# Optimization experiments

Measured on AMD Instinct MI355X. Metric: run time of the kernel, lower is better.

Reference implementation:

```python
import jax, jax.numpy as jnp
import numpy as np

B, N, D, H, DH, DEPTH = 4, 1024, 1024, 16, 64, 4
FI = int(D * 4.0 * 2 / 3)  # 2730, GEGLU inner dim
EPS = 1.1920929e-07  # torch float32 eps (RMSNorm default)
NEG = -jnp.finfo(jnp.float32).max


def rms(x, w):
    return x * jax.lax.rsqrt(jnp.mean(x * x, axis=-1, keepdims=True) + EPS) * w


def rope(t):
    # t: [b, h, n, d]; interleaved-pair rotary (lucidrains rotary_embedding_torch)
    n, d = t.shape[-2], t.shape[-1]
    inv_freq = 1.0 / (10000.0 ** (jnp.arange(0, d, 2, dtype=jnp.float32) / d))
    ang = jnp.arange(n, dtype=jnp.float32)[:, None] * inv_freq  # [n, d/2]
    cos = jnp.repeat(jnp.cos(ang), 2, axis=-1)  # [n, d]
    sin = jnp.repeat(jnp.sin(ang), 2, axis=-1)
    x = t.reshape(t.shape[:-1] + (d // 2, 2))
    rot = jnp.stack([-x[..., 1], x[..., 0]], axis=-1).reshape(t.shape)
    return t * cos + rot * sin


def setup_inputs() -> dict:
    key = jax.random.key(0)
    ks = jax.random.split(key, 14)
    s = 0.02
    return {
        "x": jax.random.normal(ks[0], (B, N, D), dtype=jnp.float32),
        "norm_attn_w": jnp.ones((DEPTH, D), jnp.float32),
        "wq": jax.random.normal(ks[1], (DEPTH, H * DH, D), jnp.float32) * s,
        "wkv": jax.random.normal(ks[2], (DEPTH, 2 * H * DH, D), jnp.float32) * s,
        "wo": jax.random.normal(ks[3], (DEPTH, D, H * DH), jnp.float32) * s,
        "wg": jax.random.normal(ks[4], (DEPTH, H, D), jnp.float32) * s,
        "wmix": jax.random.normal(ks[5], (DEPTH, H, D), jnp.float32) * s,
        "norm_ff_w": jnp.ones((DEPTH, D), jnp.float32),
        "ff_norm_w": jnp.ones((DEPTH, D), jnp.float32),
        "w_in": jax.random.normal(ks[6], (DEPTH, 2 * FI, D), jnp.float32) * s,
        "b_in": jnp.zeros((DEPTH, 2 * FI), jnp.float32),
        "w_out": jax.random.normal(ks[7], (DEPTH, D, FI), jnp.float32) * s,
        "b_out": jnp.zeros((DEPTH, D), jnp.float32),
        "final_norm_w": jnp.ones((D,), jnp.float32),
    }


def _forward(x, norm_attn_w, wq, wkv, wo, wg, wmix, norm_ff_w, ff_norm_w,
             w_in, b_in, w_out, b_out, final_norm_w):
    scale = DH ** -0.5
    causal = jnp.triu(jnp.ones((N, N), bool), k=1)  # True = masked
    value_residual = None
    for i in range(DEPTH):
        # --- attention block (pre-RMSNorm wrapper) ---
        h = rms(x, norm_attn_w[i])  # [b, n, d]
        q = jnp.einsum('bnd,ed->bne', h, wq[i]) * scale
        kv = jnp.einsum('bnd,ed->bne', h, wkv[i])
        k, v = jnp.split(kv, 2, axis=-1)
        split = lambda t: t.reshape(B, N, H, DH).transpose(0, 2, 1, 3)  # b h n d
        q, k, v = split(q), split(k), split(v)
        orig_v = v
        if value_residual is not None:
            mix = jax.nn.sigmoid(jnp.einsum('bnd,hd->bhn', h, wmix[i]))[..., None]
            v = v + mix * (value_residual - v)  # lerp(v, value_residual, mix)
        q, k = rope(q), rope(k)
        sim = jnp.einsum('bhid,bhjd->bhij', q, k)
        sim = jnp.where(causal, NEG, sim)
        attn = jax.nn.softmax(sim, axis=-1)
        out = jnp.einsum('bhij,bhjd->bhid', attn, v)
        gates = jax.nn.sigmoid(jnp.einsum('bnd,hd->bhn', h, wg[i]))[..., None]
        out = out * gates
        out = out.transpose(0, 2, 1, 3).reshape(B, N, H * DH)
        x = x + jnp.einsum('bne,de->bnd', out, wo[i])
        if value_residual is None:
            value_residual = orig_v
        # --- feedforward block (wrapper norm + FF's own pre-rmsnorm) ---
        g = rms(x, norm_ff_w[i])
        g = rms(g, ff_norm_w[i])
        u = jnp.einsum('bnd,ed->bne', g, w_in[i]) + b_in[i]
        a, gt = jnp.split(u, 2, axis=-1)
        u = a * jax.nn.gelu(gt, approximate=False)
        x = x + jnp.einsum('bnf,df->bnd', u, w_out[i]) + b_out[i]
    return rms(x, final_norm_w)


def reference(x, norm_attn_w, wq, wkv, wo, wg, wmix, norm_ff_w, ff_norm_w,
              w_in, b_in, w_out, b_out, final_norm_w):
    return _forward(x, norm_attn_w, wq, wkv, wo, wg, wmix, norm_ff_w,
                    ff_norm_w, w_in, b_in, w_out, b_out, final_norm_w)
```

## Files before the change

kernel.cpp:

```cpp
#include <hip/hip_runtime.h>
#include <cstdint>
#include <cstddef>


#define DEV_INLINE __device__ __forceinline__

typedef short bf16x8 __attribute__((ext_vector_type(8)));
typedef float f32x4 __attribute__((ext_vector_type(4)));

constexpr int Bsz = 4, Nseq = 1024, Dm = 1024, Hh = 16, DH = 64, NDEPTH = 4;
constexpr int FI = 2730;
constexpr int FI_PAD = 2752;
constexpr int FI_TILE = 2816;
constexpr int WIDE = 2 * FI_TILE;
constexpr int ROWS = Bsz * Nseq;
constexpr float EPSR = 1.1920929e-07f;

DEV_INLINE float bf2f(unsigned short u) {
  unsigned int x = ((unsigned int)u) << 16;
  float f; __builtin_memcpy(&f, &x, 4); return f;
}
DEV_INLINE unsigned short f2bf(float f) {
  unsigned int x; __builtin_memcpy(&x, &f, 4);
  unsigned int r = x + 0x7fffu + ((x >> 16) & 1u);
  return (unsigned short)(r >> 16);
}

using gptr_t = const __attribute__((address_space(1))) void*;
using lptr_t = __attribute__((address_space(3))) void*;
DEV_INLINE void gl_lds16(const void* g, void* l) {
  __builtin_amdgcn_global_load_lds((gptr_t)g, (lptr_t)l, 16, 0, 0);
}
DEV_INLINE void fence_mem() { asm volatile("" ::: "memory"); }

__global__ __launch_bounds__(256)
void convf2b(const float* __restrict__ src, unsigned short* __restrict__ dst,
             int src_rows, int src_cols, int dst_cols) {
  const int r = blockIdx.y;
  const int c8 = (blockIdx.x * blockDim.x + threadIdx.x) * 8;
  if (c8 >= dst_cols) return;
  alignas(16) unsigned short o[8];
  if (r < src_rows && c8 + 8 <= src_cols) {
    const float2* p = (const float2*)&src[(size_t)r * src_cols + c8];
    const float2 v0 = p[0], v1 = p[1], v2 = p[2], v3 = p[3];
    o[0] = f2bf(v0.x); o[1] = f2bf(v0.y); o[2] = f2bf(v1.x); o[3] = f2bf(v1.y);
    o[4] = f2bf(v2.x); o[5] = f2bf(v2.y); o[6] = f2bf(v3.x); o[7] = f2bf(v3.y);
  } else {
#pragma unroll
    for (int j = 0; j < 8; ++j) {
      const int c = c8 + j;
      float v = (r < src_rows && c < src_cols) ? src[(size_t)r * src_cols + c] : 0.0f;
      o[j] = f2bf(v);
    }
  }
  *(uint4*)&dst[(size_t)r * dst_cols + c8] = *(const uint4*)o;
}

__global__ __launch_bounds__(128)
void convf2b_g16(const float* __restrict__ src, unsigned short* __restrict__ dst) {
  const int p = blockIdx.y;
  const int c8 = threadIdx.x * 8;
  const int t = p >> 5, r5 = p & 31;
  const int srow = t * 16 + (r5 & 15);
  alignas(16) unsigned short o[8];
  if (srow < FI) {
    const size_t base = ((size_t)((r5 < 16) ? 0 : 1) * FI + srow) * 1024 + c8;
    const float4 v0 = *(const float4*)&src[base];
    const float4 v1 = *(const float4*)&src[base + 4];
    o[0]=f2bf(v0.x); o[1]=f2bf(v0.y); o[2]=f2bf(v0.z); o[3]=f2bf(v0.w);
    o[4]=f2bf(v1.x); o[5]=f2bf(v1.y); o[6]=f2bf(v1.z); o[7]=f2bf(v1.w);
  } else {
#pragma unroll
    for (int j = 0; j < 8; ++j) o[j] = 0;
  }
  *(uint4*)&dst[(size_t)p * 1024 + c8] = *(const uint4*)o;
}

__global__ __launch_bounds__(256)
void rope_tables(float* __restrict__ cost, float* __restrict__ sint) {
  int idx = blockIdx.x * 256 + threadIdx.x;
  if (idx >= Nseq * 32) return;
  int n = idx >> 5, p = idx & 31;
  float freq = powf(10000.0f, -(float)(2 * p) * (1.0f / 64.0f));
  float ang = (float)n * freq;
  cost[idx] = cosf(ang);
  sint[idx] = sinf(ang);
}

__global__ __launch_bounds__(256)
void rms_one(const float* __restrict__ x, const float* __restrict__ w,
             unsigned short* __restrict__ out) {
  __shared__ float sred[4];
  const int row = blockIdx.x, tid = threadIdx.x;
  const float4 v = ((const float4*)(x + (size_t)row * Dm))[tid];
  float ss = v.x * v.x + v.y * v.y + v.z * v.z + v.w * v.w;
#pragma unroll
  for (int o = 32; o >= 1; o >>= 1) ss += __shfl_xor(ss, o, 64);
  if ((tid & 63) == 0) sred[tid >> 6] = ss;
  __syncthreads();
  float rs = rsqrtf((sred[0] + sred[1] + sred[2] + sred[3]) * (1.0f / Dm) + EPSR);
  const float4 wv = ((const float4*)w)[tid];
  alignas(8) unsigned short o4[4] = { f2bf(v.x * rs * wv.x), f2bf(v.y * rs * wv.y),
                                      f2bf(v.z * rs * wv.z), f2bf(v.w * rs * wv.w) };
  *(uint2*)&out[(size_t)row * Dm + tid * 4] = *(const uint2*)o4;
}

__global__ __launch_bounds__(256)
void rms_ff(const float* __restrict__ x, const float* __restrict__ w1,
            const float* __restrict__ w2, unsigned short* __restrict__ out) {
  __shared__ float sred[4];
  const int row = blockIdx.x, tid = threadIdx.x;
  const float4 v = ((const float4*)(x + (size_t)row * Dm))[tid];
  const float4 w1v = ((const float4*)w1)[tid];
  const float4 w2v = ((const float4*)w2)[tid];
  float ss = v.x * v.x + v.y * v.y + v.z * v.z + v.w * v.w;
#pragma unroll
  for (int o = 32; o >= 1; o >>= 1) ss += __shfl_xor(ss, o, 64);
  if ((tid & 63) == 0) sred[tid >> 6] = ss;
  __syncthreads();
  float rs1 = rsqrtf((sred[0] + sred[1] + sred[2] + sred[3]) * (1.0f / Dm) + EPSR);
  float t0 = v.x * rs1 * w1v.x, t1 = v.y * rs1 * w1v.y;
  float t2 = v.z * rs1 * w1v.z, t3 = v.w * rs1 * w1v.w;
  float ss2 = t0 * t0 + t1 * t1 + t2 * t2 + t3 * t3;
#pragma unroll
  for (int o = 32; o >= 1; o >>= 1) ss2 += __shfl_xor(ss2, o, 64);
  __syncthreads();
  if ((tid & 63) == 0) sred[tid >> 6] = ss2;
  __syncthreads();
  float rs2 = rsqrtf((sred[0] + sred[1] + sred[2] + sred[3]) * (1.0f / Dm) + EPSR);
  alignas(8) unsigned short o4[4] = { f2bf(t0 * rs2 * w2v.x), f2bf(t1 * rs2 * w2v.y),
                                      f2bf(t2 * rs2 * w2v.z), f2bf(t3 * rs2 * w2v.w) };
  *(uint2*)&out[(size_t)row * Dm + tid * 4] = *(const uint2*)o4;
}

__global__ __launch_bounds__(256)
void rms_final(const float* __restrict__ x, const float* __restrict__ w,
               float* __restrict__ out) {
  __shared__ float sred[4];
  const int row = blockIdx.x, tid = threadIdx.x;
  const float4 v = ((const float4*)(x + (size_t)row * Dm))[tid];
  float ss = v.x * v.x + v.y * v.y + v.z * v.z + v.w * v.w;
#pragma unroll
  for (int o = 32; o >= 1; o >>= 1) ss += __shfl_xor(ss, o, 64);
  if ((tid & 63) == 0) sred[tid >> 6] = ss;
  __syncthreads();
  float rs = rsqrtf((sred[0] + sred[1] + sred[2] + sred[3]) * (1.0f / Dm) + EPSR);
  const float4 wv = ((const float4*)w)[tid];
  float4 o;
  o.x = v.x * rs * wv.x; o.y = v.y * rs * wv.y;
  o.z = v.z * rs * wv.z; o.w = v.w * rs * wv.w;
  ((float4*)(out + (size_t)row * Dm))[tid] = o;
}

template <int MODE>
__global__ __launch_bounds__(256)
void gemm_nt(const unsigned short* __restrict__ A,
             const unsigned short* __restrict__ Bw,
             void* __restrict__ Cout,
             const float* __restrict__ bias,
             const float* __restrict__ resid,
             int K, int ldc, int n_store) {
  __shared__ unsigned short As[2][128 * 64];
  __shared__ unsigned short Bs[2][128 * 64];
  const int tid = threadIdx.x;
  const int m0 = blockIdx.x * 128;
  const int n0 = blockIdx.y * 128;
  const int w = tid >> 6, l = tid & 63;
  const int wm = (w >> 1) * 64, wn = (w & 1) * 64;
  const int lr = l & 15, lg = l >> 4;
  const int lsub = l & 7, lrow8 = l >> 3;
  const int colsw = (lsub ^ lrow8) << 3;
  const unsigned short* gA = &A[(size_t)(m0 + w * 8 + lrow8) * K + colsw];
  const unsigned short* gB = &Bw[(size_t)(n0 + w * 8 + lrow8) * K + colsw];
  const size_t rstep = (size_t)32 * K;
  f32x4 acc[4][4] = {};

  auto stage = [&](int buf, int kt) {
    const int o = kt * 64;
#pragma unroll
    for (int i = 0; i < 4; ++i) {
      gl_lds16(gA + i * rstep + o, &As[buf][i * 2048 + w * 512]);
      gl_lds16(gB + i * rstep + o, &Bs[buf][i * 2048 + w * 512]);
    }
  };
  auto compute = [&](int buf) {
    bf16x8 af[2][4], bfr[2][4];
#pragma unroll
    for (int ks = 0; ks < 2; ++ks) {
      const int slot = (ks * 4 + lg) ^ (lr & 7);
#pragma unroll
      for (int fj = 0; fj < 4; ++fj)
        bfr[ks][fj] = *(const bf16x8*)&Bs[buf][(wn + fj * 16 + lr) * 64 + slot * 8];
#pragma unroll
      for (int fi = 0; fi < 4; ++fi)
        af[ks][fi] = *(const bf16x8*)&As[buf][(wm + fi * 16 + lr) * 64 + slot * 8];
    }
    __builtin_amdgcn_s_setprio(1);
#pragma unroll
    for (int ks = 0; ks < 2; ++ks)
#pragma unroll
      for (int fi = 0; fi < 4; ++fi)
#pragma unroll
        for (int fj = 0; fj < 4; ++fj)
          acc[fi][fj] = __builtin_amdgcn_mfma_f32_16x16x32_bf16(af[ks][fi], bfr[ks][fj], acc[fi][fj], 0, 0, 0);
    __builtin_amdgcn_s_setprio(0);
  };

  const int nk = K >> 6;
  stage(0, 0);
  asm volatile("s_waitcnt vmcnt(0)" ::: "memory");
  __builtin_amdgcn_s_barrier();
  fence_mem();
  int cur = 0;
#pragma unroll 1
  for (int kt = 0; kt < nk; ++kt) {
    const bool more = (kt + 1 < nk);
    if (more) stage(cur ^ 1, kt + 1);
    compute(cur);
    if (more) {
      asm volatile("s_waitcnt vmcnt(0)" ::: "memory");
      __builtin_amdgcn_s_barrier();
      fence_mem();
    }
    cur ^= 1;
  }

#pragma unroll
  for (int fi = 0; fi < 4; ++fi) {
    const int rowb = m0 + wm + fi * 16 + lg * 4;
#pragma unroll
    for (int fj = 0; fj < 4; ++fj) {
      const int col = n0 + wn + fj * 16 + lr;
#pragma unroll
      for (int r = 0; r < 4; ++r) {
        const float val = acc[fi][fj][r];
        const int rr = rowb + r;
        if constexpr (MODE == 1) {
          if (col < n_store)
            ((float*)Cout)[(size_t)rr * ldc + col] = 1.0f / (1.0f + __expf(-val));
        } else {
          const float bv = bias ? bias[col] : 0.0f;
          ((float*)Cout)[(size_t)rr * ldc + col] =
              resid[(size_t)rr * ldc + col] + val + bv;
        }
      }
    }
  }
}

template <int MODE>
__global__ __launch_bounds__(512, 2)
void gemm_nt256(const unsigned short* __restrict__ A,
                const unsigned short* __restrict__ Bw,
                void* __restrict__ Cout,
                const float* __restrict__ bias,
                int K, int ldc, int nm, int nn) {
  __shared__ unsigned short As[2][256 * 64];
  __shared__ unsigned short Bs[2][256 * 64];
  const int tid = threadIdx.x;
  const int nwg = nm * nn;
  const int qq = nwg >> 3;
  const int xcd = blockIdx.x & 7, orig = blockIdx.x >> 3;
  const int wgid = xcd * qq + orig;
  const int m0 = (wgid % nm) * 256;
  const int n0 = (wgid / nm) * 256;
  const int w = tid >> 6, l = tid & 63;
  const int wm = (w >> 2) * 128, wn = (w & 3) * 64;
  const int lr = l & 15, lg = l >> 4;
  const int lsub = l & 7, lrow8 = l >> 3;
  const int colsw = (lsub ^ lrow8) << 3;
  const unsigned short* gA = &A[(size_t)(m0 + w * 8 + lrow8) * K + colsw];
  const unsigned short* gB = &Bw[(size_t)(n0 + w * 8 + lrow8) * K + colsw];
  const size_t rstep = (size_t)64 * K;
  f32x4 acc[8][4] = {};

  auto stage_part = [&](int buf, int kt, int part) {
    const int o = kt * 64;
    const int i0 = (part & 1) * 2;
    if (part < 2) {
      gl_lds16(gA + (size_t)i0 * rstep + o,       &As[buf][i0 * 4096 + w * 512]);
      gl_lds16(gA + (size_t)(i0 + 1) * rstep + o, &As[buf][(i0 + 1) * 4096 + w * 512]);
    } else {
      gl_lds16(gB + (size_t)i0 * rstep + o,       &Bs[buf][i0 * 4096 + w * 512]);
      gl_lds16(gB + (size_t)(i0 + 1) * rstep + o, &Bs[buf][(i0 + 1) * 4096 + w * 512]);
    }
  };

  const int nk = K >> 6;
  stage_part(0, 0, 0); stage_part(0, 0, 1);
  stage_part(0, 0, 2); stage_part(0, 0, 3);
  asm volatile("s_waitcnt vmcnt(0)" ::: "memory");
  __builtin_amdgcn_s_barrier();
  fence_mem();

#pragma unroll 1
  for (int t = 0; t < nk; ++t) {
    const int p = t & 1;
    const bool more = (t + 1 < nk);
    bf16x8 bfr[4];
#pragma unroll
    for (int q = 0; q < 4; ++q) {
      const int ks = q >> 1, half = q & 1;
      const int slot = (ks * 4 + lg) ^ (lr & 7);
      if (half == 0) {
#pragma unroll
        for (int fj = 0; fj < 4; ++fj)
          bfr[fj] = *(const bf16x8*)&Bs[p][(wn + fj * 16 + lr) * 64 + slot * 8];
      }
      bf16x8 af[4];
#pragma unroll
      for (int fi = 0; fi < 4; ++fi)
        af[fi] = *(const bf16x8*)&As[p][(wm + half * 64 + fi * 16 + lr) * 64 + slot * 8];
      if (more) stage_part(p ^ 1, t + 1, q);
      __builtin_amdgcn_s_setprio(1);
#pragma unroll
      for (int fi = 0; fi < 4; ++fi)
#pragma unroll
        for (int fj = 0; fj < 4; ++fj)
          acc[half * 4 + fi][fj] =
              __builtin_amdgcn_mfma_f32_16x16x32_bf16(af[fi], bfr[fj], acc[half * 4 + fi][fj], 0, 0, 0);
      __builtin_amdgcn_s_setprio(0);
      if (q < 3) {
        __builtin_amdgcn_s_barrier();
        fence_mem();
      }
    }
    if (more) {
      asm volatile("s_waitcnt vmcnt(0)" ::: "memory");
      __builtin_amdgcn_s_barrier();
      fence_mem();
    }
  }

#pragma unroll
  for (int fi = 0; fi < 8; ++fi) {
    const int rowb = m0 + wm + fi * 16 + lg * 4;
    if constexpr (MODE == 0) {
#pragma unroll
      for (int fj = 0; fj < 4; ++fj) {
        const int col = n0 + wn + fj * 16 + lr;
#pragma unroll
        for (int r = 0; r < 4; ++r)
          ((unsigned short*)Cout)[(size_t)(rowb + r) * ldc + col] = f2bf(acc[fi][fj][r]);
      }
    } else {
#pragma unroll
      for (int fjp = 0; fjp < 2; ++fjp) {
        const int ucol = ((n0 + wn) >> 1) + fjp * 16 + lr;
        if (ucol >= FI_PAD) continue;
        const bool live = (ucol < FI);
        const float ba = live ? bias[ucol] : 0.0f;
        const float bg = live ? bias[FI + ucol] : 0.0f;
#pragma unroll
        for (int r = 0; r < 4; ++r) {
          const float va = acc[fi][2 * fjp][r] + ba;
          const float vg = acc[fi][2 * fjp + 1][r] + bg;
          const float gel = 0.5f * vg * (1.0f + erff(vg * 0.70710678118654752f));
          ((unsigned short*)Cout)[(size_t)(rowb + r) * ldc + ucol] =
              f2bf(live ? va * gel : 0.0f);
        }
      }
    }
  }
}

__global__ __launch_bounds__(256)
void rope_qk(const unsigned short* __restrict__ qkv_lin,
             const float* __restrict__ cost, const float* __restrict__ sint,
             unsigned short* __restrict__ qb, unsigned short* __restrict__ kb) {
  const int nt = blockIdx.x, bh = blockIdx.y;
  const int b = bh >> 4, h = bh & 15;
  const int tid = threadIdx.x;
  const int pi = tid & 31, r0 = tid >> 5;
  const float scale = 0.125f;
#pragma unroll
  for (int j = 0; j < 8; ++j) {
    const int n = nt * 64 + r0 + j * 8;
    const int nf = b * Nseq + n;
    const float c = cost[n * 32 + pi], s = sint[n * 32 + pi];
    const unsigned short* qp = &qkv_lin[(size_t)nf * 3072 + h * 64 + pi * 2];
    float q0 = bf2f(qp[0]), q1 = bf2f(qp[1]);
    alignas(4) unsigned short oq[2];
    oq[0] = f2bf((q0 * c - q1 * s) * scale);
    oq[1] = f2bf((q1 * c + q0 * s) * scale);
    *(unsigned int*)&qb[((size_t)bh * Nseq + n) * 64 + pi * 2] = *(const unsigned int*)oq;
    const unsigned short* kp = &qkv_lin[(size_t)nf * 3072 + 1024 + h * 64 + pi * 2];
    float k0 = bf2f(kp[0]), k1 = bf2f(kp[1]);
    alignas(4) unsigned short ok[2];
    ok[0] = f2bf(k0 * c - k1 * s);
    ok[1] = f2bf(k1 * c + k0 * s);
    *(unsigned int*)&kb[((size_t)bh * Nseq + n) * 64 + pi * 2] = *(const unsigned int*)ok;
  }
}

__global__ __launch_bounds__(256)
void v_mix_pack(const unsigned short* __restrict__ qkv_lin,
                const float* __restrict__ gm,
                unsigned short* __restrict__ vres,
                unsigned short* __restrict__ vtb, int layer) {
  __shared__ unsigned short T[64][72];
  const int nt = blockIdx.x, bh = blockIdx.y;
  const int b = bh >> 4, h = bh & 15;
  const int tid = threadIdx.x;
#pragma unroll
  for (int p = 0; p < 2; ++p) {
    int c = tid + p * 256;
    int nl = c >> 3, cg = (c & 7) << 3;
    int n = nt * 64 + nl, nf = b * Nseq + n;
    uint4 vv = *(const uint4*)&qkv_lin[(size_t)nf * 3072 + 2048 + h * 64 + cg];
    if (layer == 0) {
      *(uint4*)&vres[((size_t)bh * Nseq + n) * 64 + cg] = vv;
      *(uint4*)&T[nl][cg] = vv;
    } else {
      alignas(16) unsigned short ve[8]; *(uint4*)ve = vv;
      uint4 rv = *(const uint4*)&vres[((size_t)bh * Nseq + n) * 64 + cg];
      alignas(16) unsigned short re[8]; *(uint4*)re = rv;
      const float mix = gm[(size_t)nf * 32 + 16 + h];
      alignas(16) unsigned short oe[8];
#pragma unroll
      for (int j = 0; j < 8; ++j) {
        float v = bf2f(ve[j]), rr = bf2f(re[j]);
        oe[j] = f2bf(v + mix * (rr - v));
      }
      *(uint4*)&T[nl][cg] = *(const uint4*)oe;
    }
  }
  __syncthreads();
#pragma unroll
  for (int p = 0; p < 2; ++p) {
    int c = tid + p * 256;
    int d = c >> 3, ng = (c & 7) << 3;
    alignas(16) unsigned short oe[8];
#pragma unroll
    for (int j = 0; j < 8; ++j) oe[j] = T[ng + j][d];
    *(uint4*)&vtb[(size_t)bh * 65536 + (size_t)d * Nseq + nt * 64 + ng] = *(const uint4*)oe;
  }
}

__global__ __launch_bounds__(256)
void attn_fwd(const unsigned short* __restrict__ qb,
              const unsigned short* __restrict__ kb,
              const unsigned short* __restrict__ vtb,
              const float* __restrict__ gm,
              unsigned short* __restrict__ attn_out) {
  __shared__ unsigned short Ks[2][64 * 64];
  __shared__ unsigned short Vs[2][64 * 64];
  __shared__ unsigned short Ps[4][16][72];
  const int bid = blockIdx.x;
  const int x = bid & 7, rest = bid >> 3;
  const int bh = x * 8 + (rest & 7);
  const int qt = 15 - (rest >> 3);
  const int b = bh >> 4, h = bh & 15;
  const int tid = threadIdx.x;
  const int w = tid >> 6, l = tid & 63;
  const int lr = l & 15, lg = l >> 4;
  const int q0 = qt * 64 + w * 16;
  const size_t head = (size_t)bh * Nseq * DH;
  const int lrow8 = l >> 3;
  const int colsw = ((l & 7) ^ lrow8) << 3;

  auto stageKV = [&](int buf, int kt) {
    const int kv0 = kt * 64;
#pragma unroll
    for (int i = 0; i < 2; ++i) {
      const int rb = w * 16 + i * 8;
      gl_lds16(&kb[head + (size_t)(kv0 + rb + lrow8) * DH + colsw],
               &Ks[buf][rb * 64]);
      gl_lds16(&vtb[head + (size_t)(rb + lrow8) * Nseq + kv0 + colsw],
               &Vs[buf][rb * 64]);
    }
  };

  bf16x8 aq[2];
  aq[0] = *(const bf16x8*)&qb[head + (size_t)(q0 + lr) * DH + lg * 8];
  aq[1] = *(const bf16x8*)&qb[head + (size_t)(q0 + lr) * DH + 32 + lg * 8];

  float mrow[4] = {-1e30f, -1e30f, -1e30f, -1e30f};
  float lsum[4] = {0.f, 0.f, 0.f, 0.f};
  f32x4 acco[4] = {};

  stageKV(0, 0);
  asm volatile("s_waitcnt vmcnt(0)" ::: "memory");
  __builtin_amdgcn_s_barrier();
  fence_mem();

#pragma unroll 1
  for (int kt = 0; kt <= qt; ++kt) {
    const int p = kt & 1;
    const int kv0 = kt * 64;
    const bool more = (kt < qt);
    if (more) stageKV(p ^ 1, kt + 1);
    f32x4 s[4];
#pragma unroll
    for (int t = 0; t < 4; ++t) {
      const int krow = t * 16 + lr;
      bf16x8 bk0 = *(const bf16x8*)&Ks[p][krow * 64 + ((0 + lg) ^ (lr & 7)) * 8];
      bf16x8 bk1 = *(const bf16x8*)&Ks[p][krow * 64 + ((4 + lg) ^ (lr & 7)) * 8];
      f32x4 z = {};
      z = __builtin_amdgcn_mfma_f32_16x16x32_bf16(aq[0], bk0, z, 0, 0, 0);
      z = __builtin_amdgcn_mfma_f32_16x16x32_bf16(aq[1], bk1, z, 0, 0, 0);
      s[t] = z;
    }
    const bool diag = (kt == qt);
    float mx4[4];
    bool need = false;
#pragma unroll
    for (int r = 0; r < 4; ++r) {
      const int qr = q0 + lg * 4 + r;
      float mx = -1e30f;
#pragma unroll
      for (int t = 0; t < 4; ++t) {
        float sv = s[t][r];
        if (diag && (kv0 + t * 16 + lr > qr)) sv = -1e30f;
        s[t][r] = sv;
        mx = fmaxf(mx, sv);
      }
      mx = fmaxf(mx, __shfl_xor(mx, 1, 64));
      mx = fmaxf(mx, __shfl_xor(mx, 2, 64));
      mx = fmaxf(mx, __shfl_xor(mx, 4, 64));
      mx = fmaxf(mx, __shfl_xor(mx, 8, 64));
      mx4[r] = mx;
      need = need || (mx > mrow[r] + 8.0f);
    }
    if (__any(need)) {
#pragma unroll
      for (int r = 0; r < 4; ++r) {
        const float mn = fmaxf(mrow[r], mx4[r]);
        const float alpha = __expf(mrow[r] - mn);
        mrow[r] = mn;
        lsum[r] *= alpha;
#pragma unroll
        for (int dt = 0; dt < 4; ++dt) acco[dt][r] *= alpha;
      }
    }
#pragma unroll
    for (int r = 0; r < 4; ++r) {
      float rs = 0.f;
#pragma unroll
      for (int t = 0; t < 4; ++t) {
        float pv = __expf(s[t][r] - mrow[r]);
        s[t][r] = pv;
        rs += pv;
      }
      rs += __shfl_xor(rs, 1, 64);
      rs += __shfl_xor(rs, 2, 64);
      rs += __shfl_xor(rs, 4, 64);
      rs += __shfl_xor(rs, 8, 64);
      lsum[r] += rs;
    }
#pragma unroll
    for (int t = 0; t < 4; ++t)
#pragma unroll
      for (int r = 0; r < 4; ++r)
        Ps[w][lg * 4 + r][t * 16 + lr] = f2bf(s[t][r]);
#pragma unroll
    for (int ks = 0; ks < 2; ++ks) {
      bf16x8 ap = *(const bf16x8*)&Ps[w][lr][ks * 32 + lg * 8];
#pragma unroll
      for (int dt = 0; dt < 4; ++dt) {
        const int vrow = dt * 16 + lr;
        bf16x8 bv = *(const bf16x8*)&Vs[p][vrow * 64 + ((ks * 4 + lg) ^ (lr & 7)) * 8];
        acco[dt] = __builtin_amdgcn_mfma_f32_16x16x32_bf16(ap, bv, acco[dt], 0, 0, 0);
      }
    }
    if (more) {
      asm volatile("s_waitcnt vmcnt(0)" ::: "memory");
      __builtin_amdgcn_s_barrier();
      fence_mem();
    }
  }

#pragma unroll
  for (int r = 0; r < 4; ++r) {
    const int qr = q0 + lg * 4 + r;
    const int nf = b * Nseq + qr;
    const float gate = gm[(size_t)nf * 32 + h];
    const float inv = 1.0f / lsum[r];
#pragma unroll
    for (int dt = 0; dt < 4; ++dt)
      attn_out[(size_t)nf * Dm + h * DH + dt * 16 + lr] = f2bf(acco[dt][r] * inv * gate);
  }
}

extern "C" void kernel_launch(void* const* d_in, const int* in_sizes, int n_in,
                              void* d_out, int out_size, void* d_ws, size_t ws_size,
                              hipStream_t stream) {
  const float* x_in  = (const float*)d_in[0];
  const float* naw   = (const float*)d_in[1];
  const float* wq    = (const float*)d_in[2];
  const float* wkv   = (const float*)d_in[3];
  const float* wo    = (const float*)d_in[4];
  const float* wg    = (const float*)d_in[5];
  const float* wmix  = (const float*)d_in[6];
  const float* nfw   = (const float*)d_in[7];
  const float* ffw   = (const float*)d_in[8];
  const float* w_in  = (const float*)d_in[9];
  const float* b_in  = (const float*)d_in[10];
  const float* w_out = (const float*)d_in[11];
  const float* b_out = (const float*)d_in[12];
  const float* fnw   = (const float*)d_in[13];

  uint8_t* ws = (uint8_t*)d_ws;
  size_t off = 0;
  auto alloc = [&](size_t bytes) -> void* {
    void* p = ws + off;
    off += (bytes + 255) & ~(size_t)255;
    return p;
  };
  float*          x_res    = (float*)alloc((size_t)ROWS * Dm * 4);
  unsigned short* h        = (unsigned short*)alloc((size_t)ROWS * Dm * 2);
  unsigned short* qkv_lin  = (unsigned short*)alloc((size_t)ROWS * 3072 * 2);
  float*          gm       = (float*)alloc((size_t)ROWS * 32 * 4);
  unsigned short* qb       = (unsigned short*)alloc((size_t)64 * Nseq * DH * 2);
  unsigned short* kb       = (unsigned short*)alloc((size_t)64 * Nseq * DH * 2);
  unsigned short* vtb      = (unsigned short*)alloc((size_t)64 * Nseq * DH * 2);
  unsigned short* vres     = (unsigned short*)alloc((size_t)64 * Nseq * DH * 2);
  unsigned short* attn     = (unsigned short*)alloc((size_t)ROWS * Dm * 2);
  float*          cost     = (float*)alloc((size_t)Nseq * 32 * 4);
  float*          sint     = (float*)alloc((size_t)Nseq * 32 * 4);
  unsigned short* wqkv_bf  = (unsigned short*)alloc((size_t)3072 * 1024 * 2);
  unsigned short* wo_bf    = (unsigned short*)alloc((size_t)1024 * 1024 * 2);
  unsigned short* wgm_bf   = (unsigned short*)alloc((size_t)128 * 1024 * 2);
  unsigned short* win_bf   = (unsigned short*)alloc((size_t)WIDE * 1024 * 2);
  unsigned short* wout_bf  = (unsigned short*)alloc((size_t)1024 * FI_PAD * 2);
  unsigned short* u = qkv_lin;

  hipMemcpyAsync(x_res, x_in, (size_t)ROWS * Dm * 4, hipMemcpyDeviceToDevice, stream);
  rope_tables<<<128, 256, 0, stream>>>(cost, sint);

  for (int i = 0; i < NDEPTH; ++i) {
    convf2b<<<dim3(1, 1024), 128, 0, stream>>>(wq + (size_t)i * 1024 * 1024, wqkv_bf, 1024, 1024, 1024);
    convf2b<<<dim3(1, 2048), 128, 0, stream>>>(wkv + (size_t)i * 2048 * 1024, wqkv_bf + (size_t)1024 * 1024, 2048, 1024, 1024);
    convf2b<<<dim3(1, 1024), 128, 0, stream>>>(wo + (size_t)i * 1024 * 1024, wo_bf, 1024, 1024, 1024);
    convf2b<<<dim3(1, 16), 128, 0, stream>>>(wg + (size_t)i * 16 * 1024, wgm_bf, 16, 1024, 1024);
    convf2b<<<dim3(1, 16), 128, 0, stream>>>(wmix + (size_t)i * 16 * 1024, wgm_bf + 16 * 1024, 16, 1024, 1024);
    convf2b<<<dim3(1, 96), 128, 0, stream>>>(wg, wgm_bf + 32 * 1024, 0, 1024, 1024);
    convf2b_g16<<<dim3(1, WIDE), 128, 0, stream>>>(w_in + (size_t)i * 2 * FI * 1024, win_bf);
    convf2b<<<dim3(2, 1024), 256, 0, stream>>>(w_out + (size_t)i * 1024 * FI, wout_bf, 1024, FI, FI_PAD);

    rms_one<<<ROWS, 256, 0, stream>>>(x_res, naw + i * 1024, h);
    gemm_nt256<0><<<192, 512, 0, stream>>>(h, wqkv_bf, qkv_lin, nullptr, 1024, 3072, 16, 12);
    gemm_nt<1><<<dim3(32, 1), 256, 0, stream>>>(h, wgm_bf, gm, nullptr, nullptr, 1024, 32, 32);
    rope_qk<<<dim3(16, 64), 256, 0, stream>>>(qkv_lin, cost, sint, qb, kb);
    v_mix_pack<<<dim3(16, 64), 256, 0, stream>>>(qkv_lin, gm, vres, vtb, i);
    attn_fwd<<<1024, 256, 0, stream>>>(qb, kb, vtb, gm, attn);
    gemm_nt<2><<<dim3(32, 8), 256, 0, stream>>>(attn, wo_bf, x_res, nullptr, x_res, 1024, 1024, 1024);
    rms_ff<<<ROWS, 256, 0, stream>>>(x_res, nfw + i * 1024, ffw + i * 1024, h);
    gemm_nt256<3><<<352, 512, 0, stream>>>(h, win_bf, u, b_in + (size_t)i * 2 * FI, 1024, FI_PAD, 16, 22);
    gemm_nt<2><<<dim3(32, 8), 256, 0, stream>>>(u, wout_bf, x_res, b_out + i * 1024, x_res, FI_PAD, 1024, 1024);
  }
  rms_final<<<ROWS, 256, 0, stream>>>(x_res, fnw, (float*)d_out);
}
```

Baseline: 1.338 ms.

## Use dedicated 128x256-tile GEGLU GEMM and drop intra-loop barriers in gemm_nt256

Adds a new gemm_geglu128 kernel with 128x256 tiles and simple double-buffered staging for the FF input projection plus GEGLU epilogue. It launches 704 workgroups instead of 352, to even out the tail across CUs. gemm_nt256 loses its GEGLU epilogue and the per-quarter barriers inside its k-loop, which cuts sync stalls in the QKV GEMM. Removing those barriers risks an LDS race between staging and reading. The new kernel's ~96KB of LDS per block may also prevent the requested two blocks per CU.

```diff
diff --git a/kernel.cpp b/kernel.cpp
--- a/kernel.cpp
+++ b/kernel.cpp
@@ -320,10 +320,6 @@
           acc[half * 4 + fi][fj] =
               __builtin_amdgcn_mfma_f32_16x16x32_bf16(af[fi], bfr[fj], acc[half * 4 + fi][fj], 0, 0, 0);
       __builtin_amdgcn_s_setprio(0);
-      if (q < 3) {
-        __builtin_amdgcn_s_barrier();
-        fence_mem();
-      }
     }
     if (more) {
       asm volatile("s_waitcnt vmcnt(0)" ::: "memory");
@@ -335,30 +331,106 @@
 #pragma unroll
   for (int fi = 0; fi < 8; ++fi) {
     const int rowb = m0 + wm + fi * 16 + lg * 4;
-    if constexpr (MODE == 0) {
-#pragma unroll
-      for (int fj = 0; fj < 4; ++fj) {
-        const int col = n0 + wn + fj * 16 + lr;
-#pragma unroll
-        for (int r = 0; r < 4; ++r)
-          ((unsigned short*)Cout)[(size_t)(rowb + r) * ldc + col] = f2bf(acc[fi][fj][r]);
-      }
-    } else {
-#pragma unroll
-      for (int fjp = 0; fjp < 2; ++fjp) {
-        const int ucol = ((n0 + wn) >> 1) + fjp * 16 + lr;
-        if (ucol >= FI_PAD) continue;
-        const bool live = (ucol < FI);
-        const float ba = live ? bias[ucol] : 0.0f;
-        const float bg = live ? bias[FI + ucol] : 0.0f;
-#pragma unroll
-        for (int r = 0; r < 4; ++r) {
-          const float va = acc[fi][2 * fjp][r] + ba;
-          const float vg = acc[fi][2 * fjp + 1][r] + bg;
-          const float gel = 0.5f * vg * (1.0f + erff(vg * 0.70710678118654752f));
-          ((unsigned short*)Cout)[(size_t)(rowb + r) * ldc + ucol] =
-              f2bf(live ? va * gel : 0.0f);
-        }
+#pragma unroll
+    for (int fj = 0; fj < 4; ++fj) {
+      const int col = n0 + wn + fj * 16 + lr;
+#pragma unroll
+      for (int r = 0; r < 4; ++r)
+        ((unsigned short*)Cout)[(size_t)(rowb + r) * ldc + col] = f2bf(acc[fi][fj][r]);
+    }
+  }
+}
+
+__global__ __launch_bounds__(512, 2)
+void gemm_geglu128(const unsigned short* __restrict__ A,
+                   const unsigned short* __restrict__ Bw,
+                   unsigned short* __restrict__ Cout,
+                   const float* __restrict__ bias,
+                   int K, int ldc, int nm, int nn) {
+  __shared__ unsigned short As[2][128 * 64];
+  __shared__ unsigned short Bs[2][256 * 64];
+  const int tid = threadIdx.x;
+  const int nwg = nm * nn;
+  const int qq = nwg >> 3;
+  const int xcd = blockIdx.x & 7, orig = blockIdx.x >> 3;
+  const int wgid = xcd * qq + orig;
+  const int m0 = (wgid % nm) * 128;
+  const int n0 = (wgid / nm) * 256;
+  const int w = tid >> 6, l = tid & 63;
+  const int wm = (w >> 2) * 64, wn = (w & 3) * 64;
+  const int lr = l & 15, lg = l >> 4;
+  const int lsub = l & 7, lrow8 = l >> 3;
+  const int colsw = (lsub ^ lrow8) << 3;
+  const unsigned short* gA = &A[(size_t)(m0 + w * 8 + lrow8) * K + colsw];
+  const unsigned short* gB = &Bw[(size_t)(n0 + w * 8 + lrow8) * K + colsw];
+  const size_t rstep = (size_t)64 * K;
+  f32x4 acc[4][4] = {};
+
+  auto stage = [&](int buf, int kt) {
+    const int o = kt * 64;
+#pragma unroll
+    for (int i = 0; i < 2; ++i)
+      gl_lds16(gA + (size_t)i * rstep + o, &As[buf][i * 4096 + w * 512]);
+#pragma unroll
+    for (int i = 0; i < 4; ++i)
+      gl_lds16(gB + (size_t)i * rstep + o, &Bs[buf][i * 4096 + w * 512]);
+  };
+  auto compute = [&](int buf) {
+#pragma unroll
+    for (int ks = 0; ks < 2; ++ks) {
+      const int slot = (ks * 4 + lg) ^ (lr & 7);
+      bf16x8 bfr[4], af[4];
+#pragma unroll
+      for (int fj = 0; fj < 4; ++fj)
+        bfr[fj] = *(const bf16x8*)&Bs[buf][(wn + fj * 16 + lr) * 64 + slot * 8];
+#pragma unroll
+      for (int fi = 0; fi < 4; ++fi)
+        af[fi] = *(const bf16x8*)&As[buf][(wm + fi * 16 + lr) * 64 + slot * 8];
+      __builtin_amdgcn_s_setprio(1);
+#pragma unroll
+      for (int fi = 0; fi < 4; ++fi)
+#pragma unroll
+        for (int fj = 0; fj < 4; ++fj)
+          acc[fi][fj] = __builtin_amdgcn_mfma_f32_16x16x32_bf16(af[fi], bfr[fj], acc[fi][fj], 0, 0, 0);
+      __builtin_amdgcn_s_setprio(0);
+    }
+  };
+
+  const int nk = K >> 6;
+  stage(0, 0);
+  asm volatile("s_waitcnt vmcnt(0)" ::: "memory");
+  __builtin_amdgcn_s_barrier();
+  fence_mem();
+  int cur = 0;
+#pragma unroll 1
+  for (int kt = 0; kt < nk; ++kt) {
+    const bool more = (kt + 1 < nk);
+    if (more) stage(cur ^ 1, kt + 1);
+    compute(cur);
+    if (more) {
+      asm volatile("s_waitcnt vmcnt(0)" ::: "memory");
+      __builtin_amdgcn_s_barrier();
+      fence_mem();
+    }
+    cur ^= 1;
+  }
+
+#pragma unroll
+  for (int fi = 0; fi < 4; ++fi) {
+    const int rowb = m0 + wm + fi * 16 + lg * 4;
+#pragma unroll
+    for (int fjp = 0; fjp < 2; ++fjp) {
+      const int ucol = ((n0 + wn) >> 1) + fjp * 16 + lr;
+      if (ucol >= FI_PAD) continue;
+      const bool live = (ucol < FI);
+      const float ba = live ? bias[ucol] : 0.0f;
+      const float bg = live ? bias[FI + ucol] : 0.0f;
+#pragma unroll
+      for (int r = 0; r < 4; ++r) {
+        const float va = acc[fi][2 * fjp][r] + ba;
+        const float vg = acc[fi][2 * fjp + 1][r] + bg;
+        const float gel = 0.5f * vg * (1.0f + erff(vg * 0.70710678118654752f));
+        Cout[(size_t)(rowb + r) * ldc + ucol] = f2bf(live ? va * gel : 0.0f);
       }
     }
   }
@@ -646,7 +718,7 @@
     attn_fwd<<<1024, 256, 0, stream>>>(qb, kb, vtb, gm, attn);
     gemm_nt<2><<<dim3(32, 8), 256, 0, stream>>>(attn, wo_bf, x_res, nullptr, x_res, 1024, 1024, 1024);
     rms_ff<<<ROWS, 256, 0, stream>>>(x_res, nfw + i * 1024, ffw + i * 1024, h);
-    gemm_nt256<3><<<352, 512, 0, stream>>>(h, win_bf, u, b_in + (size_t)i * 2 * FI, 1024, FI_PAD, 16, 22);
+    gemm_geglu128<<<704, 512, 0, stream>>>(h, win_bf, u, b_in + (size_t)i * 2 * FI, 1024, FI_PAD, 32, 22);
     gemm_nt<2><<<dim3(32, 8), 256, 0, stream>>>(u, wout_bf, x_res, b_out + i * 1024, x_res, FI_PAD, 1024, 1024);
   }
   rms_final<<<ROWS, 256, 0, stream>>>(x_res, fnw, (float*)d_out);
```

New measurement: 1.300 ms. 1.03x faster.
